# Performance work log

Measured on AMD Instinct MI355X. Metric: run time of the kernel, lower is better.

Reference implementation:

```python
import jax, jax.numpy as jnp
import numpy as np

B, N, E, D, H = 8, 5000, 160000, 64, 128  # batch, nodes, edges, gnn hidden, head hidden


def _w(key, shape, scale=0.05):
    return jax.random.normal(key, shape, jnp.float32) * scale


def setup_inputs() -> dict:
    key = jax.random.key(0)
    ks = jax.random.split(key, 24)
    inp = {
        "x": jax.random.normal(ks[0], (B, N), jnp.float32),
        "edges": jax.random.randint(ks[1], (E, 2), 0, N, dtype=jnp.int32),
        "emb": _w(ks[2], (N, D)),
        # conv1: prepare FFN (2 layers, no bias, elu), update FFN (2 layers, bias)
        "c1_pw1": _w(ks[3], (D, D)), "c1_pw2": _w(ks[4], (D, D)),
        "c1_uw1": _w(ks[5], (2 * D, D)), "c1_ub1": jnp.zeros((D,), jnp.float32),
        "c1_uw2": _w(ks[6], (D, D)), "c1_ub2": jnp.zeros((D,), jnp.float32),
        # conv2
        "c2_pw1": _w(ks[7], (D, D)), "c2_pw2": _w(ks[8], (D, D)),
        "c2_uw1": _w(ks[9], (2 * D, D)), "c2_ub1": jnp.zeros((D,), jnp.float32),
        "c2_uw2": _w(ks[10], (D, D)), "c2_ub2": jnp.zeros((D,), jnp.float32),
        # TARnet prob heads: flatten -> Dense(H, elu) -> Dense(2) (mu, log_sigma)
        "w0a": _w(ks[11], (N * D, H), 0.005), "b0a": jnp.zeros((H,), jnp.float32),
        "w0b": _w(ks[12], (H, 2)), "b0b": jnp.zeros((2,), jnp.float32),
        "w1a": _w(ks[13], (N * D, H), 0.005), "b1a": jnp.zeros((H,), jnp.float32),
        "w1b": _w(ks[14], (H, 2)), "b1b": jnp.zeros((2,), jnp.float32),
    }
    return inp


def _graph_conv(h, edges, pw1, pw2, uw1, ub1, uw2, ub2):
    # h: [B, N, D]; edges: [E, 2] (parent, node)
    parents = jnp.take(h, edges[:, 0], axis=1)            # [B, E, D] gather
    m = jax.nn.elu(parents @ pw1)                          # prepare FFN (no bias)
    m = jax.nn.elu(m @ pw2)
    agg = jnp.zeros_like(h).at[:, edges[:, 1]].add(m)      # unsorted_segment_sum -> [B, N, D]
    hcat = jnp.concatenate([h, agg], axis=-1)              # combination_type='concat'
    u = jax.nn.elu(hcat @ uw1 + ub1)                       # update FFN
    return u @ uw2 + ub2                                   # final_activation=None


def reference(x, edges, emb,
              c1_pw1, c1_pw2, c1_uw1, c1_ub1, c1_uw2, c1_ub2,
              c2_pw1, c2_pw2, c2_uw1, c2_ub1, c2_uw2, c2_ub2,
              w0a, b0a, w0b, b0b, w1a, b1a, w1b, b1b):
    # node features scale learned per-node embeddings -> [B, N, D]
    h = x[:, :, None] * emb[None, :, :]
    h = _graph_conv(h, edges, c1_pw1, c1_pw2, c1_uw1, c1_ub1, c1_uw2, c1_ub2)
    h = _graph_conv(h, edges, c2_pw1, c2_pw2, c2_uw1, c2_ub1, c2_uw2, c2_ub2)
    phi = h.reshape(h.shape[0], -1)                        # flatten [B, N*D]
    y0 = jax.nn.elu(phi @ w0a + b0a) @ w0b + b0b           # [B, 2] (mu, log_sigma)
    y1 = jax.nn.elu(phi @ w1a + b1a) @ w1b + b1b           # [B, 2]
    return jnp.concatenate([y0, y1], axis=1)               # [B, 4]
```

## Files before the change

kernel.cpp:

```cpp
#include <hip/hip_runtime.h>


constexpr int B = 8, N = 5000, E = 160000, D = 64, H = 128;
constexpr int BN = B * N;
constexpr int ND = N * D;
constexpr long BND = (long)BN * D;
constexpr int KC = 640;

__device__ __forceinline__ float elu_f(float x) {
    return x > 0.0f ? x : __expf(x) - 1.0f;
}

__global__ __launch_bounds__(256) void k_count(const int* __restrict__ edges,
                                               int* __restrict__ cnt) {
    int i = blockIdx.x * 256 + threadIdx.x;
    if (i < E) atomicAdd(&cnt[edges[2 * i + 1]], 1);
}

__global__ __launch_bounds__(256) void k_scan(const int* __restrict__ cnt,
                                              int* __restrict__ offs) {
    __shared__ int part[256];
    int t = threadIdx.x;
    const int CH = 20;
    int base = t * CH;
    int s = 0;
    for (int i = 0; i < CH; ++i) { int idx = base + i; if (idx < N) s += cnt[idx]; }
    part[t] = s;
    __syncthreads();
    for (int off = 1; off < 256; off <<= 1) {
        int add = (t >= off) ? part[t - off] : 0;
        __syncthreads();
        part[t] += add;
        __syncthreads();
    }
    int run = part[t] - s;
    for (int i = 0; i < CH; ++i) {
        int idx = base + i;
        if (idx < N) { offs[idx] = run; run += cnt[idx]; }
    }
    if (t == 255) offs[N] = run;
}

__global__ __launch_bounds__(256) void k_fill(const int* __restrict__ edges,
                                              const int* __restrict__ offs,
                                              int* __restrict__ cursor,
                                              int* __restrict__ elist) {
    int i = blockIdx.x * 256 + threadIdx.x;
    if (i < E) {
        int child = edges[2 * i + 1];
        int pos = offs[child] + atomicAdd(&cursor[child], 1);
        elist[pos] = edges[2 * i];
    }
}

__global__ __launch_bounds__(512) void k_prepare(const float* __restrict__ xsrc,
                                                 const float* __restrict__ emb,
                                                 const float* __restrict__ hin,
                                                 const float* __restrict__ W1,
                                                 const float* __restrict__ W2,
                                                 float* __restrict__ M,
                                                 float* __restrict__ hwt) {
    __shared__ float sW1[64 * 64];
    __shared__ float sP[128 * 65];
    int t = threadIdx.x;
    int r0 = blockIdx.x * 128;
    for (int i = t; i < 4096; i += 512) sW1[i] = W1[i];
    if (xsrc) {
        for (int i = t; i < 128 * 64; i += 512) {
            int r = i >> 6, c = i & 63;
            int row = r0 + r;
            float v = 0.0f;
            if (row < BN) {
                int n = row % N;
                v = xsrc[row] * emb[n * 64 + c];
                hwt[(long)row * 64 + c] = v;
            }
            sP[r * 65 + c] = v;
        }
    } else {
        for (int i = t; i < 128 * 64; i += 512) {
            int r = i >> 6, c = i & 63;
            int row = r0 + r;
            sP[r * 65 + c] = (row < BN) ? hin[(long)row * 64 + c] : 0.0f;
        }
    }
    __syncthreads();

    int cg = t & 15, rg = t >> 4;
    float acc[4][4] = {};
    #pragma unroll 4
    for (int k = 0; k < 64; ++k) {
        float a[4];
        #pragma unroll
        for (int i = 0; i < 4; ++i) a[i] = sP[(rg * 4 + i) * 65 + k];
        float4 bb = *reinterpret_cast<const float4*>(&sW1[k * 64 + cg * 4]);
        #pragma unroll
        for (int i = 0; i < 4; ++i) {
            acc[i][0] += a[i] * bb.x; acc[i][1] += a[i] * bb.y;
            acc[i][2] += a[i] * bb.z; acc[i][3] += a[i] * bb.w;
        }
    }
    __syncthreads();
    #pragma unroll
    for (int i = 0; i < 4; ++i)
        #pragma unroll
        for (int j = 0; j < 4; ++j)
            sP[(rg * 4 + i) * 65 + cg * 4 + j] = elu_f(acc[i][j]);
    __syncthreads();

    float acc2[4][4] = {};
    #pragma unroll 4
    for (int k = 0; k < 64; ++k) {
        float a[4];
        #pragma unroll
        for (int i = 0; i < 4; ++i) a[i] = sP[(rg * 4 + i) * 65 + k];
        float4 bb = *reinterpret_cast<const float4*>(&W2[k * 64 + cg * 4]);
        #pragma unroll
        for (int i = 0; i < 4; ++i) {
            acc2[i][0] += a[i] * bb.x; acc2[i][1] += a[i] * bb.y;
            acc2[i][2] += a[i] * bb.z; acc2[i][3] += a[i] * bb.w;
        }
    }
    #pragma unroll
    for (int i = 0; i < 4; ++i) {
        int row = r0 + rg * 4 + i;
        if (row < BN) {
            float4 o = make_float4(elu_f(acc2[i][0]), elu_f(acc2[i][1]),
                                   elu_f(acc2[i][2]), elu_f(acc2[i][3]));
            *reinterpret_cast<float4*>(&M[(long)row * 64 + cg * 4]) = o;
        }
    }
}

__global__ __launch_bounds__(256) void k_aggregate(const float* __restrict__ M,
                                                   const int* __restrict__ offs,
                                                   const int* __restrict__ elist,
                                                   float* __restrict__ agg) {
    int t = threadIdx.x;
    int lane = t & 63, wv = t >> 6;
    int bn = blockIdx.x * 4 + wv;
    int b = bn / N;
    int n = bn - b * N;
    int e0 = offs[n], e1 = offs[n + 1];
    const float* Mb = M + (long)b * ND;
    int h4 = lane & 15, le = lane >> 4;
    float4 acc = make_float4(0.f, 0.f, 0.f, 0.f);
    for (int e = e0 + le; e < e1; e += 4) {
        int p = elist[e];
        float4 v = *reinterpret_cast<const float4*>(&Mb[(long)p * 64 + h4 * 4]);
        acc.x += v.x; acc.y += v.y; acc.z += v.z; acc.w += v.w;
    }
    #pragma unroll
    for (int m = 16; m <= 32; m <<= 1) {
        acc.x += __shfl_xor(acc.x, m);
        acc.y += __shfl_xor(acc.y, m);
        acc.z += __shfl_xor(acc.z, m);
        acc.w += __shfl_xor(acc.w, m);
    }
    if (le == 0)
        *reinterpret_cast<float4*>(&agg[(long)bn * 64 + h4 * 4]) = acc;
}

__global__ __launch_bounds__(512) void k_update(const float* __restrict__ h,
                                                const float* __restrict__ agg,
                                                const float* __restrict__ W1,
                                                const float* __restrict__ b1,
                                                const float* __restrict__ W2,
                                                const float* __restrict__ b2,
                                                float* __restrict__ hout) {
    __shared__ float sW1[128 * 64];
    __shared__ float sP[64 * 129];
    int t = threadIdx.x;
    long r0 = (long)blockIdx.x * 64;
    for (int i = t; i < 128 * 64; i += 512) sW1[i] = W1[i];
    for (int i = t; i < 64 * 128; i += 512) {
        int r = i >> 7, k = i & 127;
        long row = r0 + r;
        float v = (k < 64) ? h[row * 64 + k] : agg[row * 64 + (k - 64)];
        sP[r * 129 + k] = v;
    }
    __syncthreads();

    int cg = t & 15, rg = t >> 4;
    float acc[2][4] = {};
    #pragma unroll 4
    for (int k = 0; k < 128; ++k) {
        float a0 = sP[(rg * 2 + 0) * 129 + k];
        float a1 = sP[(rg * 2 + 1) * 129 + k];
        float4 bb = *reinterpret_cast<const float4*>(&sW1[k * 64 + cg * 4]);
        acc[0][0] += a0 * bb.x; acc[0][1] += a0 * bb.y; acc[0][2] += a0 * bb.z; acc[0][3] += a0 * bb.w;
        acc[1][0] += a1 * bb.x; acc[1][1] += a1 * bb.y; acc[1][2] += a1 * bb.z; acc[1][3] += a1 * bb.w;
    }
    float4 bv1 = *reinterpret_cast<const float4*>(&b1[cg * 4]);
    __syncthreads();
    #pragma unroll
    for (int i = 0; i < 2; ++i) {
        sP[(rg * 2 + i) * 129 + cg * 4 + 0] = elu_f(acc[i][0] + bv1.x);
        sP[(rg * 2 + i) * 129 + cg * 4 + 1] = elu_f(acc[i][1] + bv1.y);
        sP[(rg * 2 + i) * 129 + cg * 4 + 2] = elu_f(acc[i][2] + bv1.z);
        sP[(rg * 2 + i) * 129 + cg * 4 + 3] = elu_f(acc[i][3] + bv1.w);
    }
    __syncthreads();

    float acc2[2][4] = {};
    #pragma unroll 4
    for (int k = 0; k < 64; ++k) {
        float a0 = sP[(rg * 2 + 0) * 129 + k];
        float a1 = sP[(rg * 2 + 1) * 129 + k];
        float4 bb = *reinterpret_cast<const float4*>(&W2[k * 64 + cg * 4]);
        acc2[0][0] += a0 * bb.x; acc2[0][1] += a0 * bb.y; acc2[0][2] += a0 * bb.z; acc2[0][3] += a0 * bb.w;
        acc2[1][0] += a1 * bb.x; acc2[1][1] += a1 * bb.y; acc2[1][2] += a1 * bb.z; acc2[1][3] += a1 * bb.w;
    }
    float4 bv2 = *reinterpret_cast<const float4*>(&b2[cg * 4]);
    #pragma unroll
    for (int i = 0; i < 2; ++i) {
        float4 o = make_float4(acc2[i][0] + bv2.x, acc2[i][1] + bv2.y,
                               acc2[i][2] + bv2.z, acc2[i][3] + bv2.w);
        *reinterpret_cast<float4*>(&hout[(r0 + rg * 2 + i) * 64 + cg * 4]) = o;
    }
}

__global__ __launch_bounds__(256) void k_head(const float* __restrict__ phi,
                                              const float* __restrict__ w0a,
                                              const float* __restrict__ w1a,
                                              float* __restrict__ hidden) {
    __shared__ float smem[8 * 32 * 33];
    const float* wa = blockIdx.y ? w1a : w0a;
    float* hid = hidden + blockIdx.y * (8 * H);
    int t = threadIdx.x;
    int k0 = blockIdx.x * KC;

    #pragma unroll
    for (int b = 0; b < 8; ++b)
        for (int kk = t; kk < KC; kk += 256)
            smem[b * KC + kk] = phi[(long)b * ND + k0 + kk];
    __syncthreads();

    int h4 = t & 31, kl = t >> 5;
    const float* wp = wa + (long)(k0 + kl) * H + h4 * 4;
    float4 acc[8];
    #pragma unroll
    for (int b = 0; b < 8; ++b) acc[b] = make_float4(0.f, 0.f, 0.f, 0.f);

    #pragma unroll 4
    for (int it = 0; it < KC / 8; ++it) {
        float4 w4 = *reinterpret_cast<const float4*>(wp + (long)it * 8 * H);
        int kk = it * 8 + kl;
        #pragma unroll
        for (int b = 0; b < 8; ++b) {
            float p = smem[b * KC + kk];
            acc[b].x += p * w4.x; acc[b].y += p * w4.y;
            acc[b].z += p * w4.z; acc[b].w += p * w4.w;
        }
    }
    __syncthreads();

    int base = (kl * 32 + h4) * 33;
    #pragma unroll
    for (int b = 0; b < 8; ++b) {
        smem[base + b * 4 + 0] = acc[b].x;
        smem[base + b * 4 + 1] = acc[b].y;
        smem[base + b * 4 + 2] = acc[b].z;
        smem[base + b * 4 + 3] = acc[b].w;
    }
    __syncthreads();

    int rh4 = t & 31, rb = t >> 5;
    float s0 = 0.f, s1 = 0.f, s2 = 0.f, s3 = 0.f;
    #pragma unroll
    for (int klr = 0; klr < 8; ++klr) {
        int idx = (klr * 32 + rh4) * 33 + rb * 4;
        s0 += smem[idx + 0]; s1 += smem[idx + 1];
        s2 += smem[idx + 2]; s3 += smem[idx + 3];
    }
    unsafeAtomicAdd(&hid[rb * H + rh4 * 4 + 0], s0);
    unsafeAtomicAdd(&hid[rb * H + rh4 * 4 + 1], s1);
    unsafeAtomicAdd(&hid[rb * H + rh4 * 4 + 2], s2);
    unsafeAtomicAdd(&hid[rb * H + rh4 * 4 + 3], s3);
}

__global__ __launch_bounds__(64) void k_final(const float* __restrict__ hidden,
                                              const float* __restrict__ b0a,
                                              const float* __restrict__ w0b,
                                              const float* __restrict__ b0b,
                                              const float* __restrict__ b1a,
                                              const float* __restrict__ w1b,
                                              const float* __restrict__ b1b,
                                              float* __restrict__ out) {
    int t = threadIdx.x;
    if (t >= 32) return;
    int head = t >> 4, b = (t >> 1) & 7, j = t & 1;
    const float* hid = hidden + head * (8 * H) + b * H;
    const float* ba = head ? b1a : b0a;
    const float* wb = head ? w1b : w0b;
    const float* bb = head ? b1b : b0b;
    float acc = 0.0f;
    for (int hh = 0; hh < H; ++hh)
        acc += elu_f(hid[hh] + ba[hh]) * wb[hh * 2 + j];
    out[b * 4 + head * 2 + j] = acc + bb[j];
}

extern "C" void kernel_launch(void* const* d_in, const int* in_sizes, int n_in,
                              void* d_out, int out_size, void* d_ws, size_t ws_size,
                              hipStream_t stream) {
    const float* x      = (const float*)d_in[0];
    const int*   edges  = (const int*)d_in[1];
    const float* emb    = (const float*)d_in[2];
    const float* c1_pw1 = (const float*)d_in[3];
    const float* c1_pw2 = (const float*)d_in[4];
    const float* c1_uw1 = (const float*)d_in[5];
    const float* c1_ub1 = (const float*)d_in[6];
    const float* c1_uw2 = (const float*)d_in[7];
    const float* c1_ub2 = (const float*)d_in[8];
    const float* c2_pw1 = (const float*)d_in[9];
    const float* c2_pw2 = (const float*)d_in[10];
    const float* c2_uw1 = (const float*)d_in[11];
    const float* c2_ub1 = (const float*)d_in[12];
    const float* c2_uw2 = (const float*)d_in[13];
    const float* c2_ub2 = (const float*)d_in[14];
    const float* w0a    = (const float*)d_in[15];
    const float* b0a    = (const float*)d_in[16];
    const float* w0b    = (const float*)d_in[17];
    const float* b0b    = (const float*)d_in[18];
    const float* w1a    = (const float*)d_in[19];
    const float* b1a    = (const float*)d_in[20];
    const float* w1b    = (const float*)d_in[21];
    const float* b1b    = (const float*)d_in[22];
    float* out = (float*)d_out;

    float* hA     = (float*)d_ws;
    float* hB     = hA + BND;
    float* Mu     = hB + BND;
    float* agg    = Mu + BND;
    float* hidden = agg + BND;
    int* cnt      = (int*)(hidden + 2048);
    int* cursor   = cnt + N;
    int* offs     = cursor + N;
    int* elist    = offs + N + 1;

    hipMemsetAsync(hidden, 0, (2048 + 2 * N) * sizeof(float), stream);

    k_count<<<(E + 255) / 256, 256, 0, stream>>>(edges, cnt);
    k_scan<<<1, 256, 0, stream>>>(cnt, offs);
    k_fill<<<(E + 255) / 256, 256, 0, stream>>>(edges, offs, cursor, elist);

    k_prepare<<<(BN + 127) / 128, 512, 0, stream>>>(x, emb, nullptr, c1_pw1, c1_pw2, Mu, hA);
    k_aggregate<<<BN / 4, 256, 0, stream>>>(Mu, offs, elist, agg);
    k_update<<<BN / 64, 512, 0, stream>>>(hA, agg, c1_uw1, c1_ub1, c1_uw2, c1_ub2, hB);

    k_prepare<<<(BN + 127) / 128, 512, 0, stream>>>(nullptr, emb, hB, c2_pw1, c2_pw2, Mu, nullptr);
    k_aggregate<<<BN / 4, 256, 0, stream>>>(Mu, offs, elist, agg);
    k_update<<<BN / 64, 512, 0, stream>>>(hB, agg, c2_uw1, c2_ub1, c2_uw2, c2_ub2, hA);

    k_head<<<dim3(ND / KC, 2), 256, 0, stream>>>(hA, w0a, w1a, hidden);
    k_final<<<1, 64, 0, stream>>>(hidden, b0a, w0b, b0b, b1a, w1b, b1b, out);
}
```

Measured before the change: 651.5 us.

## Halve head K-chunk, software-prefetch weights, and reduce wave halves via shuffle

The head GEMV kernel now uses K chunks of 320, which doubles the number of blocks and halves shared memory per block. The weight float4 loads are software-pipelined with a 4-deep register buffer so the next group of loads is issued before the current FMAs. Partial sums from the two halves of each 64-lane wavefront are combined with __shfl_xor, so the shared-memory reduction covers 4 waves instead of 8 k-lanes. The goal is better latency hiding on the bandwidth-bound 2x82MB weight stream, at the cost of twice as many atomic adds into the hidden buffer.

```diff
diff --git a/kernel.cpp b/kernel.cpp
--- a/kernel.cpp
+++ b/kernel.cpp
@@ -5,7 +5,8 @@
 constexpr int BN = B * N;
 constexpr int ND = N * D;
 constexpr long BND = (long)BN * D;
-constexpr int KC = 640;
+constexpr int KC = 320;
+constexpr int NIT = KC / 8;
 
 __device__ __forceinline__ float elu_f(float x) {
     return x > 0.0f ? x : __expf(x) - 1.0f;
@@ -224,7 +225,7 @@
                                               const float* __restrict__ w0a,
                                               const float* __restrict__ w1a,
                                               float* __restrict__ hidden) {
-    __shared__ float smem[8 * 32 * 33];
+    __shared__ float smem[4 * 32 * 33];
     const float* wa = blockIdx.y ? w1a : w0a;
     float* hid = hidden + blockIdx.y * (8 * H);
     int t = threadIdx.x;
@@ -236,47 +237,80 @@
             smem[b * KC + kk] = phi[(long)b * ND + k0 + kk];
     __syncthreads();
 
-    int h4 = t & 31, kl = t >> 5;
+    int w = t >> 6, l = t & 63;
+    int h4 = l & 31, kh = l >> 5;
+    int kl = w * 2 + kh;
     const float* wp = wa + (long)(k0 + kl) * H + h4 * 4;
+
     float4 acc[8];
     #pragma unroll
     for (int b = 0; b < 8; ++b) acc[b] = make_float4(0.f, 0.f, 0.f, 0.f);
-
-    #pragma unroll 4
-    for (int it = 0; it < KC / 8; ++it) {
-        float4 w4 = *reinterpret_cast<const float4*>(wp + (long)it * 8 * H);
-        int kk = it * 8 + kl;
+    float4 buf[4];
+    #pragma unroll
+    for (int j = 0; j < 4; ++j)
+        buf[j] = *reinterpret_cast<const float4*>(wp + (long)j * 8 * H);
+
+    for (int g = 0; g < NIT / 4 - 1; ++g) {
+        #pragma unroll
+        for (int j = 0; j < 4; ++j) {
+            float4 w4 = buf[j];
+            buf[j] = *reinterpret_cast<const float4*>(wp + (long)((g + 1) * 4 + j) * 8 * H);
+            int kk = (g * 4 + j) * 8 + kl;
+            #pragma unroll
+            for (int b = 0; b < 8; ++b) {
+                float p = smem[b * KC + kk];
+                acc[b].x += p * w4.x; acc[b].y += p * w4.y;
+                acc[b].z += p * w4.z; acc[b].w += p * w4.w;
+            }
+        }
+    }
+    {
+        const int g = NIT / 4 - 1;
+        #pragma unroll
+        for (int j = 0; j < 4; ++j) {
+            float4 w4 = buf[j];
+            int kk = (g * 4 + j) * 8 + kl;
+            #pragma unroll
+            for (int b = 0; b < 8; ++b) {
+                float p = smem[b * KC + kk];
+                acc[b].x += p * w4.x; acc[b].y += p * w4.y;
+                acc[b].z += p * w4.z; acc[b].w += p * w4.w;
+            }
+        }
+    }
+
+    #pragma unroll
+    for (int b = 0; b < 8; ++b) {
+        acc[b].x += __shfl_xor(acc[b].x, 32);
+        acc[b].y += __shfl_xor(acc[b].y, 32);
+        acc[b].z += __shfl_xor(acc[b].z, 32);
+        acc[b].w += __shfl_xor(acc[b].w, 32);
+    }
+    __syncthreads();
+    if (kh == 0) {
+        int base = (w * 32 + h4) * 33;
         #pragma unroll
         for (int b = 0; b < 8; ++b) {
-            float p = smem[b * KC + kk];
-            acc[b].x += p * w4.x; acc[b].y += p * w4.y;
-            acc[b].z += p * w4.z; acc[b].w += p * w4.w;
-        }
-    }
-    __syncthreads();
-
-    int base = (kl * 32 + h4) * 33;
-    #pragma unroll
-    for (int b = 0; b < 8; ++b) {
-        smem[base + b * 4 + 0] = acc[b].x;
-        smem[base + b * 4 + 1] = acc[b].y;
-        smem[base + b * 4 + 2] = acc[b].z;
-        smem[base + b * 4 + 3] = acc[b].w;
-    }
-    __syncthreads();
-
-    int rh4 = t & 31, rb = t >> 5;
+            smem[base + b * 4 + 0] = acc[b].x;
+            smem[base + b * 4 + 1] = acc[b].y;
+            smem[base + b * 4 + 2] = acc[b].z;
+            smem[base + b * 4 + 3] = acc[b].w;
+        }
+    }
+    __syncthreads();
+
+    int h4r = t & 31, br = t >> 5;
     float s0 = 0.f, s1 = 0.f, s2 = 0.f, s3 = 0.f;
     #pragma unroll
-    for (int klr = 0; klr < 8; ++klr) {
-        int idx = (klr * 32 + rh4) * 33 + rb * 4;
+    for (int wv = 0; wv < 4; ++wv) {
+        int idx = (wv * 32 + h4r) * 33 + br * 4;
         s0 += smem[idx + 0]; s1 += smem[idx + 1];
         s2 += smem[idx + 2]; s3 += smem[idx + 3];
     }
-    unsafeAtomicAdd(&hid[rb * H + rh4 * 4 + 0], s0);
-    unsafeAtomicAdd(&hid[rb * H + rh4 * 4 + 1], s1);
-    unsafeAtomicAdd(&hid[rb * H + rh4 * 4 + 2], s2);
-    unsafeAtomicAdd(&hid[rb * H + rh4 * 4 + 3], s3);
+    unsafeAtomicAdd(&hid[br * H + h4r * 4 + 0], s0);
+    unsafeAtomicAdd(&hid[br * H + h4r * 4 + 1], s1);
+    unsafeAtomicAdd(&hid[br * H + h4r * 4 + 2], s2);
+    unsafeAtomicAdd(&hid[br * H + h4r * 4 + 3], s3);
 }
 
 __global__ __launch_bounds__(64) void k_final(const float* __restrict__ hidden,
```

New measurement: 715.0 us. +9.8%, slower.
